# Kernel optimization log

Measured on AMD Instinct MI355X. Metric: run time of the kernel, lower is better.

## Reference

```python
import jax, jax.numpy as jnp
import numpy as np

TAU = 2.0        # LIF membrane time constant
ALPHA = 4.0      # spikingjelly default Sigmoid surrogate alpha
NUM_HEADS = 8

@jax.custom_vjp
def spike(x):
    return (x >= 0.0).astype(x.dtype)

def _spike_fwd(x):
    return spike(x), x

def _spike_bwd(x, g):
    s = jax.nn.sigmoid(ALPHA * x)
    return (g * ALPHA * s * (1.0 - s),)

spike.defvjp(_spike_fwd, _spike_bwd)

def lif(x_seq, v_th):
    """Multi-step LIF over leading time dim. Hard reset to 0, detach_reset."""
    def step(v, xt):
        h = v + (xt - v) / TAU
        s = spike(h - v_th)
        v_new = h * (1.0 - jax.lax.stop_gradient(s))
        return v_new, s
    _, s_seq = jax.lax.scan(step, jnp.zeros_like(x_seq[0]), x_seq)
    return s_seq

def bn_eval(x, w, b, m, v, eps=1e-5):
    # BatchNorm1d in eval mode over channel dim C (last axis here, since the
    # torch code transposes to (TB,C,N) purely to make C the channel axis).
    inv = w / jnp.sqrt(v + eps)
    return x * inv + (b - m * inv)

def setup_inputs() -> dict:
    key = jax.random.key(0)
    T, B, N, C = 4, 8, 512, 512
    ks = jax.random.split(key, 32)
    d = {"x": jax.random.normal(ks[0], (T, B, N, C), dtype=jnp.float32)}
    names = ["q", "k", "v", "p"]
    for i, nm in enumerate(names):
        kk = jax.random.split(ks[i + 1], 6)
        d[nm + "_w"] = jax.random.normal(kk[0], (C, C), dtype=jnp.float32) * (C ** -0.5)
        d[nm + "_b"] = jax.random.normal(kk[1], (C,), dtype=jnp.float32) * 0.01
        d[nm + "_bn_w"] = jax.random.uniform(kk[2], (C,), minval=0.5, maxval=1.5, dtype=jnp.float32)
        d[nm + "_bn_b"] = jax.random.normal(kk[3], (C,), dtype=jnp.float32) * 0.1
        d[nm + "_bn_m"] = jax.random.normal(kk[4], (C,), dtype=jnp.float32) * 0.1
        d[nm + "_bn_v"] = jax.random.uniform(kk[5], (C,), minval=0.5, maxval=1.5, dtype=jnp.float32)
    return d

def _forward(x, q_w, q_b, q_bn_w, q_bn_b, q_bn_m, q_bn_v,
             k_w, k_b, k_bn_w, k_bn_b, k_bn_m, k_bn_v,
             v_w, v_b, v_bn_w, v_bn_b, v_bn_m, v_bn_v,
             p_w, p_b, p_bn_w, p_bn_b, p_bn_m, p_bn_v):
    T, B, N, C = x.shape
    H = NUM_HEADS
    hd = C // H
    scale = hd ** -0.5

    def branch(w, b, bw, bb, bm, bv):
        y = jnp.einsum("tbnc,dc->tbnd", x, w) + b            # Linear
        y = bn_eval(y, bw, bb, bm, bv)                        # BN1d (eval)
        y = lif(y, 1.0)                                       # (T,B,N,C) spikes
        return y.reshape(T, B, N, H, hd).transpose(0, 1, 3, 2, 4)  # (T,B,H,N,hd)

    q = branch(q_w, q_b, q_bn_w, q_bn_b, q_bn_m, q_bn_v)
    k = branch(k_w, k_b, k_bn_w, k_bn_b, k_bn_m, k_bn_v)
    v = branch(v_w, v_b, v_bn_w, v_bn_b, v_bn_m, v_bn_v)

    gamma = 1.0 - 2.0 ** (-5.0 - jnp.arange(H, dtype=jnp.float32))
    idx = jnp.arange(N)
    dist = jnp.abs(idx[:, None] - idx[None, :]).astype(jnp.float32)  # bidirectional
    D = gamma[:, None, None] ** dist                                  # (H,N,N)

    attn = jnp.einsum("tbhnd,tbhmd->tbhnm", q, k) * scale * D
    out = jnp.einsum("tbhnm,tbhmd->tbhnd", attn, v)
    out = out.transpose(0, 1, 3, 2, 4).reshape(T, B, N, C)
    out = lif(out, 0.5)                                      # retention_lif, v_th=0.5

    y = jnp.einsum("tbnc,dc->tbnd", out, p_w) + p_b
    y = bn_eval(y, p_bn_w, p_bn_b, p_bn_m, p_bn_v)
    return lif(y, 1.0)

def reference(x, q_w, q_b, q_bn_w, q_bn_b, q_bn_m, q_bn_v,
              k_w, k_b, k_bn_w, k_bn_b, k_bn_m, k_bn_v,
              v_w, v_b, v_bn_w, v_bn_b, v_bn_m, v_bn_v,
              p_w, p_b, p_bn_w, p_bn_b, p_bn_m, p_bn_v):
    return _forward(x, q_w, q_b, q_bn_w, q_bn_b, q_bn_m, q_bn_v,
                    k_w, k_b, k_bn_w, k_bn_b, k_bn_m, k_bn_v,
                    v_w, v_b, v_bn_w, v_bn_b, v_bn_m, v_bn_v,
                    p_w, p_b, p_bn_w, p_bn_b, p_bn_m, p_bn_v)
```

## Files before the change

kernel.cpp:

```cpp
#include <hip/hip_runtime.h>
#include <cstdint>

typedef unsigned long long u64;

#define TPB 256
#define MARGIN 5e-4
#define FCAP (1 << 20)

typedef __bf16 bf16x8 __attribute__((ext_vector_type(8)));
typedef __bf16 bf16x4 __attribute__((ext_vector_type(4)));
typedef float f32x4 __attribute__((ext_vector_type(4)));

__global__ void init_kernel(double* __restrict__ pw, int* __restrict__ ctr) {
    int h = threadIdx.x;
    if (h < 8) {
        double gamma = 1.0 - ldexp(1.0, -5 - h);
        double p = 1.0;
        for (int i = 0; i < 512; ++i) { pw[h * 512 + i] = p; p *= gamma; }
        ctr[h] = 0;
    }
}

__global__ void split_all(const float* __restrict__ x,
                          const float* __restrict__ w0, const float* __restrict__ w1,
                          const float* __restrict__ w2, const float* __restrict__ w3,
                          __bf16* __restrict__ Xh, __bf16* __restrict__ Xl,
                          __bf16* __restrict__ Wsp) {
    int blk = blockIdx.x;
    if (blk < 8192) {
        size_t i = (size_t)blk * 1024 + threadIdx.x * 4;
        int m = (int)(i >> 9), c = (int)(i & 511);
        int mp = (m & 4095) * 4 + (m >> 12);
        float4 v = *(const float4*)(x + i);
        bf16x4 h4, l4;
        #pragma unroll
        for (int e = 0; e < 4; ++e) {
            float f = (&v.x)[e];
            __bf16 hh = (__bf16)f;
            h4[e] = hh;
            l4[e] = (__bf16)(f - (float)hh);
        }
        size_t dst = (size_t)mp * 512 + c;
        *(bf16x4*)(Xh + dst) = h4;
        *(bf16x4*)(Xl + dst) = l4;
    } else {
        int wb = blk - 8192;
        int br = wb >> 8;
        const float* ws[4] = {w0, w1, w2, w3};
        const float* src = ws[br];
        __bf16* hi = Wsp + (size_t)br * 524288;
        __bf16* lo = hi + 262144;
        size_t i = (size_t)(wb & 255) * 1024 + threadIdx.x * 4;
        float4 v = *(const float4*)(src + i);
        bf16x4 h4, l4;
        #pragma unroll
        for (int e = 0; e < 4; ++e) {
            float f = (&v.x)[e];
            __bf16 hh = (__bf16)f;
            h4[e] = hh;
            l4[e] = (__bf16)(f - (float)hh);
        }
        *(bf16x4*)(hi + i) = h4;
        *(bf16x4*)(lo + i) = l4;
    }
}

__global__ __launch_bounds__(256) void gemm_lif_mask(
    const __bf16* __restrict__ Ahg, const __bf16* __restrict__ Alg,
    const __bf16* __restrict__ Whg, const __bf16* __restrict__ Wlg,
    const float* __restrict__ bias,
    const float* __restrict__ bnw, const float* __restrict__ bnb,
    const float* __restrict__ bnm, const float* __restrict__ bnv,
    u64* __restrict__ msk, int* __restrict__ ctr, int* __restrict__ list, int slot)
{
    __shared__ __bf16 AhS[128][40];
    __shared__ __bf16 AlS[128][40];
    __shared__ __bf16 WhS[128][40];
    __shared__ __bf16 WlS[128][40];

    const int tid = threadIdx.x;
    const int m0 = blockIdx.x * 128;
    const int d0 = blockIdx.y * 128;
    const int wv = tid >> 6;
    const int wm = wv >> 1;
    const int wd = wv & 1;
    const int lane = tid & 63;
    const int fr = lane & 15;
    const int fg = lane >> 4;
    const int srow = tid >> 1;
    const int sseg = (tid & 1) * 16;

    f32x4 acc[4][4];
    #pragma unroll
    for (int i = 0; i < 4; ++i)
        #pragma unroll
        for (int j = 0; j < 4; ++j)
            acc[i][j] = (f32x4){0.f, 0.f, 0.f, 0.f};

    for (int k0 = 0; k0 < 512; k0 += 32) {
        __syncthreads();
        {
            const __bf16* pa = Ahg + (size_t)(m0 + srow) * 512 + k0 + sseg;
            *(bf16x8*)&AhS[srow][sseg]     = *(const bf16x8*)pa;
            *(bf16x8*)&AhS[srow][sseg + 8] = *(const bf16x8*)(pa + 8);
            const __bf16* pl = Alg + (size_t)(m0 + srow) * 512 + k0 + sseg;
            *(bf16x8*)&AlS[srow][sseg]     = *(const bf16x8*)pl;
            *(bf16x8*)&AlS[srow][sseg + 8] = *(const bf16x8*)(pl + 8);
            const __bf16* pwh = Whg + (size_t)(d0 + srow) * 512 + k0 + sseg;
            const __bf16* pwl = Wlg + (size_t)(d0 + srow) * 512 + k0 + sseg;
            *(bf16x8*)&WhS[srow][sseg]     = *(const bf16x8*)pwh;
            *(bf16x8*)&WhS[srow][sseg + 8] = *(const bf16x8*)(pwh + 8);
            *(bf16x8*)&WlS[srow][sseg]     = *(const bf16x8*)pwl;
            *(bf16x8*)&WlS[srow][sseg + 8] = *(const bf16x8*)(pwl + 8);
        }
        __syncthreads();

        bf16x8 ah[4], bh[4], bl[4];
        #pragma unroll
        for (int i = 0; i < 4; ++i)
            ah[i] = *(const bf16x8*)&AhS[wm * 64 + i * 16 + fr][fg * 8];
        #pragma unroll
        for (int j = 0; j < 4; ++j) {
            bh[j] = *(const bf16x8*)&WhS[wd * 64 + j * 16 + fr][fg * 8];
            bl[j] = *(const bf16x8*)&WlS[wd * 64 + j * 16 + fr][fg * 8];
        }
        #pragma unroll
        for (int i = 0; i < 4; ++i)
            #pragma unroll
            for (int j = 0; j < 4; ++j) {
                acc[i][j] = __builtin_amdgcn_mfma_f32_16x16x32_bf16(ah[i], bh[j], acc[i][j], 0, 0, 0);
                acc[i][j] = __builtin_amdgcn_mfma_f32_16x16x32_bf16(ah[i], bl[j], acc[i][j], 0, 0, 0);
            }
        bf16x8 al[4];
        #pragma unroll
        for (int i = 0; i < 4; ++i)
            al[i] = *(const bf16x8*)&AlS[wm * 64 + i * 16 + fr][fg * 8];
        #pragma unroll
        for (int i = 0; i < 4; ++i)
            #pragma unroll
            for (int j = 0; j < 4; ++j)
                acc[i][j] = __builtin_amdgcn_mfma_f32_16x16x32_bf16(al[i], bh[j], acc[i][j], 0, 0, 0);
    }

    double invj[4], shj[4], bsj[4];
    #pragma unroll
    for (int j = 0; j < 4; ++j) {
        int d = d0 + wd * 64 + j * 16 + fr;
        invj[j] = (double)bnw[d] / sqrt((double)bnv[d] + 1e-5);
        shj[j]  = (double)bnb[d] - (double)bnm[d] * invj[j];
        bsj[j]  = (double)bias[d];
    }
    int hword = (d0 >> 6) + wd;
    int bn0 = blockIdx.x * 32 + wm * 16;

    #pragma unroll
    for (int i = 0; i < 4; ++i) {
        int bn = bn0 + i * 4 + fg;
        int b = bn >> 9, n = bn & 511;
        u64 w[4] = {0ull, 0ull, 0ull, 0ull};
        #pragma unroll
        for (int j = 0; j < 4; ++j) {
            double v = 0.0;
            bool fl = false;
            #pragma unroll
            for (int t = 0; t < 4; ++t) {
                double y = ((double)acc[i][j][t] + bsj[j]) * invj[j] + shj[j];
                double hh = v + (y - v) * 0.5;
                fl |= fabs(hh - 1.0) < MARGIN;
                bool s = hh >= 1.0;
                u64 blt = __ballot(s);
                w[t] |= ((blt >> (fg * 16)) & 0xFFFFull) << (j * 16);
                v = s ? 0.0 : hh;
            }
            if (fl) {
                int d = d0 + wd * 64 + j * 16 + fr;
                int idx = atomicAdd(ctr + slot, 1);
                if (idx < FCAP) list[idx] = (b << 18) | (n << 9) | d;
            }
        }
        if (fr == 0) {
            #pragma unroll
            for (int t = 0; t < 4; ++t)
                msk[((t * 8 + b) * 8 + hword) * 512 + n] = w[t];
        }
    }
}

__global__ __launch_bounds__(256) void gemm_final_lif(
    const __bf16* __restrict__ Ahg,
    const __bf16* __restrict__ Whg, const __bf16* __restrict__ Wlg,
    const float* __restrict__ bias,
    const float* __restrict__ bnw, const float* __restrict__ bnb,
    const float* __restrict__ bnm, const float* __restrict__ bnv,
    float* __restrict__ out, int* __restrict__ ctr, int* __restrict__ list)
{
    __shared__ __bf16 AhS[128][40];
    __shared__ __bf16 WhS[128][40];
    __shared__ __bf16 WlS[128][40];

    const int tid = threadIdx.x;
    const int m0 = blockIdx.x * 128;
    const int d0 = blockIdx.y * 128;
    const int wv = tid >> 6;
    const int wm = wv >> 1;
    const int wd = wv & 1;
    const int lane = tid & 63;
    const int fr = lane & 15;
    const int fg = lane >> 4;
    const int srow = tid >> 1;
    const int sseg = (tid & 1) * 16;

    f32x4 acc[4][4];
    #pragma unroll
    for (int i = 0; i < 4; ++i)
        #pragma unroll
        for (int j = 0; j < 4; ++j)
            acc[i][j] = (f32x4){0.f, 0.f, 0.f, 0.f};

    for (int k0 = 0; k0 < 512; k0 += 32) {
        __syncthreads();
        {
            const __bf16* pa = Ahg + (size_t)(m0 + srow) * 512 + k0 + sseg;
            *(bf16x8*)&AhS[srow][sseg]     = *(const bf16x8*)pa;
            *(bf16x8*)&AhS[srow][sseg + 8] = *(const bf16x8*)(pa + 8);
            const __bf16* pwh = Whg + (size_t)(d0 + srow) * 512 + k0 + sseg;
            const __bf16* pwl = Wlg + (size_t)(d0 + srow) * 512 + k0 + sseg;
            *(bf16x8*)&WhS[srow][sseg]     = *(const bf16x8*)pwh;
            *(bf16x8*)&WhS[srow][sseg + 8] = *(const bf16x8*)(pwh + 8);
            *(bf16x8*)&WlS[srow][sseg]     = *(const bf16x8*)pwl;
            *(bf16x8*)&WlS[srow][sseg + 8] = *(const bf16x8*)(pwl + 8);
        }
        __syncthreads();

        bf16x8 ah[4], bh[4], bl[4];
        #pragma unroll
        for (int i = 0; i < 4; ++i)
            ah[i] = *(const bf16x8*)&AhS[wm * 64 + i * 16 + fr][fg * 8];
        #pragma unroll
        for (int j = 0; j < 4; ++j) {
            bh[j] = *(const bf16x8*)&WhS[wd * 64 + j * 16 + fr][fg * 8];
            bl[j] = *(const bf16x8*)&WlS[wd * 64 + j * 16 + fr][fg * 8];
        }
        #pragma unroll
        for (int i = 0; i < 4; ++i)
            #pragma unroll
            for (int j = 0; j < 4; ++j) {
                acc[i][j] = __builtin_amdgcn_mfma_f32_16x16x32_bf16(ah[i], bh[j], acc[i][j], 0, 0, 0);
                acc[i][j] = __builtin_amdgcn_mfma_f32_16x16x32_bf16(ah[i], bl[j], acc[i][j], 0, 0, 0);
            }
    }

    double invj[4], shj[4], bsj[4];
    #pragma unroll
    for (int j = 0; j < 4; ++j) {
        int d = d0 + wd * 64 + j * 16 + fr;
        invj[j] = (double)bnw[d] / sqrt((double)bnv[d] + 1e-5);
        shj[j]  = (double)bnb[d] - (double)bnm[d] * invj[j];
        bsj[j]  = (double)bias[d];
    }
    int bn0 = blockIdx.x * 32 + wm * 16;

    #pragma unroll
    for (int i = 0; i < 4; ++i) {
        int bn = bn0 + i * 4 + fg;
        int b = bn >> 9, n = bn & 511;
        #pragma unroll
        for (int j = 0; j < 4; ++j) {
            int d = d0 + wd * 64 + j * 16 + fr;
            double v = 0.0;
            bool fl = false;
            #pragma unroll
            for (int t = 0; t < 4; ++t) {
                double y = ((double)acc[i][j][t] + bsj[j]) * invj[j] + shj[j];
                double hh = v + (y - v) * 0.5;
                fl |= fabs(hh - 1.0) < MARGIN;
                bool s = hh >= 1.0;
                out[((size_t)((t * 8 + b) * 512 + n) << 9) + d] = s ? 1.0f : 0.0f;
                v = s ? 0.0 : hh;
            }
            if (fl) {
                int idx = atomicAdd(ctr + 3, 1);
                if (idx < FCAP) list[idx] = (b << 18) | (n << 9) | d;
            }
        }
    }
}

__global__ void fix_mask(const float* __restrict__ x, const float* __restrict__ w,
                         const float* __restrict__ bias,
                         const float* __restrict__ bnw, const float* __restrict__ bnb,
                         const float* __restrict__ bnm, const float* __restrict__ bnv,
                         u64* __restrict__ msk, const int* __restrict__ ctr,
                         const int* __restrict__ list, int slot) {
    int cnt = ctr[slot]; if (cnt > FCAP) cnt = FCAP;
    int wv = (blockIdx.x * blockDim.x + threadIdx.x) >> 6;
    int nw = (gridDim.x * blockDim.x) >> 6;
    int lane = threadIdx.x & 63;
    for (int i = wv; i < cnt; i += nw) {
        int g = list[i];
        int c = g & 511, n = (g >> 9) & 511, b = g >> 18;
        int h = c >> 6;
        const float* wr = w + (size_t)c * 512;
        double dot[4];
        #pragma unroll
        for (int t = 0; t < 4; ++t) {
            const float* xr = x + ((size_t)((t * 8 + b) * 512 + n) << 9);
            double p = 0.0;
            #pragma unroll
            for (int j = 0; j < 8; ++j)
                p += (double)xr[lane + 64 * j] * (double)wr[lane + 64 * j];
            dot[t] = p;
        }
        #pragma unroll
        for (int off = 32; off; off >>= 1) {
            #pragma unroll
            for (int t = 0; t < 4; ++t)
                dot[t] += __shfl_xor(dot[t], off, 64);
        }
        if (lane == 0) {
            double inv = (double)bnw[c] / sqrt((double)bnv[c] + 1e-5);
            double sh  = (double)bnb[c] - (double)bnm[c] * inv;
            double bs  = (double)bias[c];
            double v = 0.0;
            u64 bit = 1ull << (c & 63);
            for (int t = 0; t < 4; ++t) {
                double y = (dot[t] + bs) * inv + sh;
                double hh = v + (y - v) * 0.5;
                bool s = hh >= 1.0;
                u64* wp_ = &msk[((t * 8 + b) * 8 + h) * 512 + n];
                if (s) atomicOr(wp_, bit); else atomicAnd(wp_, ~bit);
                v = s ? 0.0 : hh;
            }
        }
    }
}

__global__ __launch_bounds__(256) void ret_fused2(
    const u64* __restrict__ qm, const u64* __restrict__ km,
    const u64* __restrict__ vm, const double* __restrict__ pw,
    float* __restrict__ O)
{
    int bid = blockIdx.x;
    int tbh = bid >> 3;
    int n0 = (bid & 7) * 64;
    int h = tbh & 7;
    int tb = tbh >> 3;
    int tid = threadIdx.x;
    int wv = tid >> 6, lane = tid & 63, fr = lane & 15, fg = lane >> 4;
    int wn = wv * 16;

    __shared__ __bf16 Ks[64][72];
    __shared__ u64 VsTg[16][66];
    __shared__ u64 ShTg[4][16][17];
    __shared__ u64 SlTg[4][16][17];
    __shared__ u64 vmc[64];
    __shared__ float pwf[512];

    int base = tbh * 512;
    for (int i = tid; i < 512; i += 256) pwf[i] = (float)pw[h * 512 + i] * 0.125f;

    union U8 { u64 q[2]; bf16x8 v; };

    u64 qw = qm[base + n0 + wn + fr];
    bf16x8 qf[2];
    #pragma unroll
    for (int ks = 0; ks < 2; ++ks) {
        int e0 = ks * 32 + fg * 8;
        u64 plo = 0, phi = 0;
        #pragma unroll
        for (int e = 0; e < 4; ++e) {
            if ((qw >> (e0 + e)) & 1ull)     plo |= 0x3F80ull << (16 * e);
            if ((qw >> (e0 + 4 + e)) & 1ull) phi |= 0x3F80ull << (16 * e);
        }
        U8 u; u.q[0] = plo; u.q[1] = phi; qf[ks] = u.v;
    }

    f32x4 acc_o[4];
    #pragma unroll
    for (int j = 0; j < 4; ++j) acc_o[j] = (f32x4){0.f, 0.f, 0.f, 0.f};

    int nglob = n0 + wn + fr;

    for (int mc = 0; mc < 8; ++mc) {
        __syncthreads();
        {
            int row = tid >> 2, q4 = (tid & 3) * 16;
            u64 kw = km[base + mc * 64 + row];
            #pragma unroll
            for (int s = 0; s < 4; ++s) {
                int e0 = q4 + s * 4;
                u64 pk = 0;
                #pragma unroll
                for (int e = 0; e < 4; ++e)
                    if ((kw >> (e0 + e)) & 1ull) pk |= 0x3F80ull << (16 * e);
                *(u64*)&Ks[row][e0] = pk;
            }
        }
        if (tid < 64) vmc[tid] = vm[base + mc * 64 + tid];
        __syncthreads();
        {
            #pragma unroll
            for (int c = 0; c < 4; ++c) {
                int mg = wv * 4 + c;
                u64 pk = 0;
                #pragma unroll
                for (int e = 0; e < 4; ++e)
                    if ((vmc[mg * 4 + e] >> lane) & 1ull) pk |= 0x3F80ull << (16 * e);
                VsTg[mg][lane] = pk;
            }
        }
        f32x4 accs[4];
        #pragma unroll
        for (int j = 0; j < 4; ++j) accs[j] = (f32x4){0.f, 0.f, 0.f, 0.f};
        #pragma unroll
        for (int ks = 0; ks < 2; ++ks) {
            #pragma unroll
            for (int j = 0; j < 4; ++j) {
                bf16x8 ka = *(const bf16x8*)&Ks[j * 16 + fr][ks * 32 + fg * 8];
                accs[j] = __builtin_amdgcn_mfma_f32_16x16x32_bf16(ka, qf[ks], accs[j], 0, 0, 0);
            }
        }
        #pragma unroll
        for (int j = 0; j < 4; ++j) {
            u64 ph = 0, pl = 0;
            #pragma unroll
            for (int reg = 0; reg < 4; ++reg) {
                int m = mc * 64 + j * 16 + fg * 4 + reg;
                int dist = nglob - m; if (dist < 0) dist = -dist;
                float a = accs[j][reg] * pwf[dist];
                __bf16 hp = (__bf16)a;
                __bf16 lp = (__bf16)(a - (float)hp);
                ph |= (u64)__builtin_bit_cast(unsigned short, hp) << (16 * reg);
                pl |= (u64)__builtin_bit_cast(unsigned short, lp) << (16 * reg);
            }
            ShTg[wv][j * 4 + fg][fr] = ph;
            SlTg[wv][j * 4 + fg][fr] = pl;
        }
        __syncthreads();
        #pragma unroll
        for (int ks2 = 0; ks2 < 2; ++ks2) {
            int mga = ks2 * 8 + fg * 2;
            U8 ua, ul;
            ua.q[0] = ShTg[wv][mga][fr];  ua.q[1] = ShTg[wv][mga + 1][fr];
            ul.q[0] = SlTg[wv][mga][fr];  ul.q[1] = SlTg[wv][mga + 1][fr];
            #pragma unroll
            for (int j2 = 0; j2 < 4; ++j2) {
                U8 uv;
                uv.q[0] = VsTg[mga][j2 * 16 + fr];
                uv.q[1] = VsTg[mga + 1][j2 * 16 + fr];
                acc_o[j2] = __builtin_amdgcn_mfma_f32_16x16x32_bf16(ua.v, uv.v, acc_o[j2], 0, 0, 0);
                acc_o[j2] = __builtin_amdgcn_mfma_f32_16x16x32_bf16(ul.v, uv.v, acc_o[j2], 0, 0, 0);
            }
        }
    }

    #pragma unroll
    for (int j2 = 0; j2 < 4; ++j2) {
        int c = h * 64 + j2 * 16 + fr;
        #pragma unroll
        for (int reg = 0; reg < 4; ++reg) {
            int n = n0 + wn + fg * 4 + reg;
            O[((size_t)(tb * 512 + n) << 9) + c] = acc_o[j2][reg];
        }
    }
}

__global__ void lif_ret_bf2(const float* __restrict__ Y, __bf16* __restrict__ Rb,
                            int* __restrict__ ctr, int* __restrict__ list) {
    int g = blockIdx.x * TPB + threadIdx.x;
    int c = g & 511, n = (g >> 9) & 511, b = g >> 18;
    size_t pbase = ((size_t)(b * 512 + n) * 4) * 512 + c;
    double v = 0.0, eb = 0.0;
    bool flag = false;
    for (int t = 0; t < 4; ++t) {
        size_t idx = ((size_t)((t * 8 + b) * 512 + n) << 9) + c;
        double x = (double)Y[idx];
        double hh = v + (x - v) * 0.5;
        eb = 0.5 * eb + 0.5 * (fabs(x) * 1e-4);
        flag |= fabs(hh - 0.5) <= eb + 1e-9;
        bool s = hh >= 0.5;
        Rb[pbase + (size_t)t * 512] = s ? (__bf16)1.0f : (__bf16)0.0f;
        v = s ? 0.0 : hh;
        if (s) eb = 0.0;
    }
    if (flag) {
        int i2 = atomicAdd(ctr + 4, 1);
        if (i2 < FCAP) list[i2] = g;
    }
}

__global__ void repair_ret_bf2(const u64* __restrict__ qm, const u64* __restrict__ km,
                               const u64* __restrict__ vm, const double* __restrict__ pw,
                               const int* __restrict__ ctr, const int* __restrict__ list,
                               __bf16* __restrict__ Rb) {
    int cnt = ctr[4]; if (cnt > FCAP) cnt = FCAP;
    int wv = (blockIdx.x * blockDim.x + threadIdx.x) >> 6;
    int nw = (gridDim.x * blockDim.x) >> 6;
    int lane = threadIdx.x & 63;
    for (int i = wv; i < cnt; i += nw) {
        int g = list[i];
        int c = g & 511, n = (g >> 9) & 511, b = g >> 18;
        int h = c >> 6, d = c & 63;
        double acc_t[4];
        for (int t = 0; t < 4; ++t) {
            int base = ((t * 8 + b) * 8 + h) * 512;
            u64 qw = qm[base + n];
            double p = 0.0;
            for (int j = 0; j < 8; ++j) {
                int m = j * 64 + lane;
                u64 kk = km[base + m];
                u64 vvm = vm[base + m];
                if ((vvm >> d) & 1ull) {
                    int dist = n - m; if (dist < 0) dist = -dist;
                    p += (double)__popcll(qw & kk) * pw[h * 512 + dist];
                }
            }
            acc_t[t] = p;
        }
        #pragma unroll
        for (int off = 32; off; off >>= 1) {
            #pragma unroll
            for (int t = 0; t < 4; ++t) acc_t[t] += __shfl_xor(acc_t[t], off, 64);
        }
        if (lane == 0) {
            double v = 0.0;
            size_t pbase = ((size_t)(b * 512 + n) * 4) * 512 + c;
            for (int t = 0; t < 4; ++t) {
                double x = acc_t[t] * 0.125;
                double hh = v + (x - v) * 0.5;
                bool s = hh >= 0.5;
                Rb[pbase + (size_t)t * 512] = s ? (__bf16)1.0f : (__bf16)0.0f;
                v = s ? 0.0 : hh;
            }
        }
    }
}

__global__ void fix_final_direct(const __bf16* __restrict__ rr, const float* __restrict__ w,
                                 const float* __restrict__ bias,
                                 const float* __restrict__ bnw, const float* __restrict__ bnb,
                                 const float* __restrict__ bnm, const float* __restrict__ bnv,
                                 const int* __restrict__ ctr, const int* __restrict__ list,
                                 float* __restrict__ out) {
    int cnt = ctr[3]; if (cnt > FCAP) cnt = FCAP;
    int wv = (blockIdx.x * blockDim.x + threadIdx.x) >> 6;
    int nw = (gridDim.x * blockDim.x) >> 6;
    int lane = threadIdx.x & 63;
    for (int i = wv; i < cnt; i += nw) {
        int g = list[i];
        int c = g & 511, n = (g >> 9) & 511, b = g >> 18;
        const float* wr = w + (size_t)c * 512;
        double dot[4];
        #pragma unroll
        for (int t = 0; t < 4; ++t) {
            const __bf16* xr = rr + ((size_t)(b * 512 + n) * 4 + t) * 512;
            double p = 0.0;
            #pragma unroll
            for (int j = 0; j < 8; ++j)
                p += (double)(float)xr[lane + 64 * j] * (double)wr[lane + 64 * j];
            dot[t] = p;
        }
        #pragma unroll
        for (int off = 32; off; off >>= 1) {
            #pragma unroll
            for (int t = 0; t < 4; ++t)
                dot[t] += __shfl_xor(dot[t], off, 64);
        }
        if (lane == 0) {
            double inv = (double)bnw[c] / sqrt((double)bnv[c] + 1e-5);
            double sh  = (double)bnb[c] - (double)bnm[c] * inv;
            double bs  = (double)bias[c];
            double v = 0.0;
            for (int t = 0; t < 4; ++t) {
                double y = (dot[t] + bs) * inv + sh;
                double hh = v + (y - v) * 0.5;
                bool s = hh >= 1.0;
                out[((size_t)((t * 8 + b) * 512 + n) << 9) + c] = s ? 1.0f : 0.0f;
                v = s ? 0.0 : hh;
            }
        }
    }
}

__global__ __launch_bounds__(256) void gemm_bn_mfma(
    const float* __restrict__ A, const float* __restrict__ W,
    const float* __restrict__ bias,
    const float* __restrict__ bnw, const float* __restrict__ bnb,
    const float* __restrict__ bnm, const float* __restrict__ bnv,
    float* __restrict__ out)
{
    __shared__ __bf16 Ah[128][36];
    __shared__ __bf16 Al[128][36];
    __shared__ __bf16 Wh[64][36];
    __shared__ __bf16 Wl[64][36];

    const int tid = threadIdx.x;
    const int m0 = blockIdx.x * 128;
    const int d0 = blockIdx.y * 64;
    const int wv = tid >> 6;
    const int wm = wv >> 1;
    const int wd = wv & 1;
    const int lane = tid & 63;
    const int fr = lane & 15;
    const int fg = lane >> 4;
    const int srow = tid >> 3;
    const int scol = (tid & 7) * 4;

    f32x4 acc[4][2];
    #pragma unroll
    for (int i = 0; i < 4; ++i)
        #pragma unroll
        for (int j = 0; j < 2; ++j)
            acc[i][j] = (f32x4){0.f, 0.f, 0.f, 0.f};

    for (int k0 = 0; k0 < 512; k0 += 32) {
        __syncthreads();
        #pragma unroll
        for (int rep = 0; rep < 4; ++rep) {
            int row = srow + 32 * rep;
            float4 va = *(const float4*)(A + (size_t)(m0 + row) * 512 + k0 + scol);
            #pragma unroll
            for (int e = 0; e < 4; ++e) {
                float f = (&va.x)[e];
                __bf16 h = (__bf16)f;
                Ah[row][scol + e] = h;
                Al[row][scol + e] = (__bf16)(f - (float)h);
            }
        }
        #pragma unroll
        for (int rep = 0; rep < 2; ++rep) {
            int row = srow + 32 * rep;
            float4 vw = *(const float4*)(W + (size_t)(d0 + row) * 512 + k0 + scol);
            #pragma unroll
            for (int e = 0; e < 4; ++e) {
                float f = (&vw.x)[e];
                __bf16 h = (__bf16)f;
                Wh[row][scol + e] = h;
                Wl[row][scol + e] = (__bf16)(f - (float)h);
            }
        }
        __syncthreads();

        union FU { bf16x8 v8; struct { __bf16 a[4], b[4]; } s; };
        bf16x8 ah[4], al[4], bh[2], bl[2];
        #pragma unroll
        for (int i = 0; i < 4; ++i) {
            int row = wm * 64 + i * 16 + fr;
            FU u1, u2;
            *(double*)&u1.s.a[0] = *(const double*)&Ah[row][fg * 8];
            *(double*)&u1.s.b[0] = *(const double*)&Ah[row][fg * 8 + 4];
            *(double*)&u2.s.a[0] = *(const double*)&Al[row][fg * 8];
            *(double*)&u2.s.b[0] = *(const double*)&Al[row][fg * 8 + 4];
            ah[i] = u1.v8; al[i] = u2.v8;
        }
        #pragma unroll
        for (int j = 0; j < 2; ++j) {
            int row = wd * 32 + j * 16 + fr;
            FU u1, u2;
            *(double*)&u1.s.a[0] = *(const double*)&Wh[row][fg * 8];
            *(double*)&u1.s.b[0] = *(const double*)&Wh[row][fg * 8 + 4];
            *(double*)&u2.s.a[0] = *(const double*)&Wl[row][fg * 8];
            *(double*)&u2.s.b[0] = *(const double*)&Wl[row][fg * 8 + 4];
            bh[j] = u1.v8; bl[j] = u2.v8;
        }
        #pragma unroll
        for (int i = 0; i < 4; ++i)
            #pragma unroll
            for (int j = 0; j < 2; ++j) {
                acc[i][j] = __builtin_amdgcn_mfma_f32_16x16x32_bf16(ah[i], bh[j], acc[i][j], 0, 0, 0);
                acc[i][j] = __builtin_amdgcn_mfma_f32_16x16x32_bf16(ah[i], bl[j], acc[i][j], 0, 0, 0);
                acc[i][j] = __builtin_amdgcn_mfma_f32_16x16x32_bf16(al[i], bh[j], acc[i][j], 0, 0, 0);
            }
    }

    #pragma unroll
    for (int j = 0; j < 2; ++j) {
        int d = d0 + wd * 32 + j * 16 + fr;
        double inv = (double)bnw[d] / sqrt((double)bnv[d] + 1e-5);
        double sh  = (double)bnb[d] - (double)bnm[d] * inv;
        double bs  = (double)bias[d];
        #pragma unroll
        for (int i = 0; i < 4; ++i) {
            #pragma unroll
            for (int reg = 0; reg < 4; ++reg) {
                int m = m0 + wm * 64 + i * 16 + fg * 4 + reg;
                out[(size_t)m * 512 + d] = (float)(((double)acc[i][j][reg] + bs) * inv + sh);
            }
        }
    }
}

__global__ void lif_mask_flag(const float* __restrict__ Y, u64* __restrict__ msk,
                              int* __restrict__ ctr, int* __restrict__ list, int slot) {
    int g = blockIdx.x * TPB + threadIdx.x;
    int c = g & 511, n = (g >> 9) & 511, b = g >> 18;
    int h = c >> 6;
    int lane = threadIdx.x & 63;
    double v = 0.0;
    bool flag = false;
    for (int t = 0; t < 4; ++t) {
        float y = Y[((size_t)((t * 8 + b) * 512 + n) << 9) + c];
        double hh = v + ((double)y - v) * 0.5;
        flag |= fabs(hh - 1.0) < MARGIN;
        bool s = hh >= 1.0;
        u64 mk = __ballot(s);
        if (lane == 0) msk[((t * 8 + b) * 8 + h) * 512 + n] = mk;
        v = s ? 0.0 : hh;
    }
    if (flag) {
        int idx = atomicAdd(ctr + slot, 1);
        if (idx < FCAP) list[idx] = g;
    }
}

__global__ void lif_ret_f(const float* __restrict__ Y, float* __restrict__ R,
                          int* __restrict__ ctr, int* __restrict__ list) {
    int g = blockIdx.x * TPB + threadIdx.x;
    int c = g & 511, n = (g >> 9) & 511, b = g >> 18;
    double v = 0.0, eb = 0.0;
    bool flag = false;
    for (int t = 0; t < 4; ++t) {
        size_t idx = ((size_t)((t * 8 + b) * 512 + n) << 9) + c;
        double x = (double)Y[idx];
        double hh = v + (x - v) * 0.5;
        eb = 0.5 * eb + 0.5 * (fabs(x) * 1e-4);
        flag |= fabs(hh - 0.5) <= eb + 1e-9;
        bool s = hh >= 0.5;
        R[idx] = s ? 1.0f : 0.0f;
        v = s ? 0.0 : hh;
        if (s) eb = 0.0;
    }
    if (flag) {
        int i2 = atomicAdd(ctr + 4, 1);
        if (i2 < FCAP) list[i2] = g;
    }
}

__global__ void repair_ret_f(const u64* __restrict__ qm, const u64* __restrict__ km,
                             const u64* __restrict__ vm, const double* __restrict__ pw,
                             const int* __restrict__ ctr, const int* __restrict__ list,
                             float* __restrict__ r) {
    int cnt = ctr[4]; if (cnt > FCAP) cnt = FCAP;
    int wv = (blockIdx.x * blockDim.x + threadIdx.x) >> 6;
    int nw = (gridDim.x * blockDim.x) >> 6;
    int lane = threadIdx.x & 63;
    for (int i = wv; i < cnt; i += nw) {
        int g = list[i];
        int c = g & 511, n = (g >> 9) & 511, b = g >> 18;
        int h = c >> 6, d = c & 63;
        double acc_t[4];
        for (int t = 0; t < 4; ++t) {
            int base = ((t * 8 + b) * 8 + h) * 512;
            u64 qw = qm[base + n];
            double p = 0.0;
            for (int j = 0; j < 8; ++j) {
                int m = j * 64 + lane;
                u64 kk = km[base + m];
                u64 vvm = vm[base + m];
                if ((vvm >> d) & 1ull) {
                    int dist = n - m; if (dist < 0) dist = -dist;
                    p += (double)__popcll(qw & kk) * pw[h * 512 + dist];
                }
            }
            acc_t[t] = p;
        }
        #pragma unroll
        for (int off = 32; off; off >>= 1) {
            #pragma unroll
            for (int t = 0; t < 4; ++t) acc_t[t] += __shfl_xor(acc_t[t], off, 64);
        }
        if (lane == 0) {
            double v = 0.0;
            for (int t = 0; t < 4; ++t) {
                double x = acc_t[t] * 0.125;
                double hh = v + (x - v) * 0.5;
                bool s = hh >= 0.5;
                r[((size_t)((t * 8 + b) * 512 + n) << 9) + c] = s ? 1.0f : 0.0f;
                v = s ? 0.0 : hh;
            }
        }
    }
}

__global__ void final_flag(const float* __restrict__ Y, int* __restrict__ ctr,
                           int* __restrict__ list) {
    int g = blockIdx.x * TPB + threadIdx.x;
    int c = g & 511, n = (g >> 9) & 511, b = g >> 18;
    double v = 0.0;
    bool flag = false;
    for (int t = 0; t < 4; ++t) {
        float y = Y[((size_t)((t * 8 + b) * 512 + n) << 9) + c];
        double hh = v + ((double)y - v) * 0.5;
        flag |= fabs(hh - 1.0) < MARGIN;
        bool s = hh >= 1.0;
        v = s ? 0.0 : hh;
    }
    if (flag) {
        int idx = atomicAdd(ctr + 3, 1);
        if (idx < FCAP) list[idx] = g;
    }
}

__global__ void fix_final_f(const float* __restrict__ rr, const float* __restrict__ w,
                            const float* __restrict__ bias,
                            const float* __restrict__ bnw, const float* __restrict__ bnb,
                            const float* __restrict__ bnm, const float* __restrict__ bnv,
                            const int* __restrict__ ctr, int* __restrict__ list) {
    int cnt = ctr[3]; if (cnt > FCAP) cnt = FCAP;
    int wv = (blockIdx.x * blockDim.x + threadIdx.x) >> 6;
    int nw = (gridDim.x * blockDim.x) >> 6;
    int lane = threadIdx.x & 63;
    for (int i = wv; i < cnt; i += nw) {
        int g = list[i] & 0x00FFFFFF;
        int c = g & 511, n = (g >> 9) & 511, b = g >> 18;
        const float* wr = w + (size_t)c * 512;
        double dot[4];
        #pragma unroll
        for (int t = 0; t < 4; ++t) {
            const float* xr = rr + ((size_t)((t * 8 + b) * 512 + n) << 9);
            double p = 0.0;
            #pragma unroll
            for (int j = 0; j < 8; ++j)
                p += (double)xr[lane + 64 * j] * (double)wr[lane + 64 * j];
            dot[t] = p;
        }
        #pragma unroll
        for (int off = 32; off; off >>= 1) {
            #pragma unroll
            for (int t = 0; t < 4; ++t)
                dot[t] += __shfl_xor(dot[t], off, 64);
        }
        if (lane == 0) {
            double inv = (double)bnw[c] / sqrt((double)bnv[c] + 1e-5);
            double sh  = (double)bnb[c] - (double)bnm[c] * inv;
            double bs  = (double)bias[c];
            double v = 0.0;
            int sp = 0;
            for (int t = 0; t < 4; ++t) {
                double y = (dot[t] + bs) * inv + sh;
                double hh = v + (y - v) * 0.5;
                bool s = hh >= 1.0;
                sp |= (s ? 1 : 0) << t;
                v = s ? 0.0 : hh;
            }
            list[i] = g | (sp << 24);
        }
    }
}

__global__ void final_write(const float* __restrict__ Y, float* __restrict__ out) {
    int g = blockIdx.x * TPB + threadIdx.x;
    int c = g & 511, n = (g >> 9) & 511, b = g >> 18;
    double v = 0.0;
    for (int t = 0; t < 4; ++t) {
        size_t idx = ((size_t)((t * 8 + b) * 512 + n) << 9) + c;
        float y = Y[idx];
        double hh = v + ((double)y - v) * 0.5;
        bool s = hh >= 1.0;
        out[idx] = s ? 1.0f : 0.0f;
        v = s ? 0.0 : hh;
    }
}

__global__ void fix_scatter(const int* __restrict__ ctr, const int* __restrict__ list,
                            float* __restrict__ out) {
    int cnt = ctr[3]; if (cnt > FCAP) cnt = FCAP;
    int i = blockIdx.x * blockDim.x + threadIdx.x;
    if (i >= cnt) return;
    int e = list[i];
    int g = e & 0x00FFFFFF, sp = (e >> 24) & 0xF;
    int c = g & 511, n = (g >> 9) & 511, b = g >> 18;
    for (int t = 0; t < 4; ++t)
        out[((size_t)((t * 8 + b) * 512 + n) << 9) + c] = ((sp >> t) & 1) ? 1.0f : 0.0f;
}

extern "C" void kernel_launch(void* const* d_in, const int* in_sizes, int n_in,
                              void* d_out, int out_size, void* d_ws, size_t ws_size,
                              hipStream_t stream) {
    const float* x = (const float*)d_in[0];
    const float *w[4], *bi[4], *bnw[4], *bnb[4], *bnm[4], *bnv[4];
    for (int br = 0; br < 4; ++br) {
        int base = 1 + br * 6;
        w[br]   = (const float*)d_in[base + 0];
        bi[br]  = (const float*)d_in[base + 1];
        bnw[br] = (const float*)d_in[base + 2];
        bnb[br] = (const float*)d_in[base + 3];
        bnm[br] = (const float*)d_in[base + 4];
        bnv[br] = (const float*)d_in[base + 5];
    }

    const size_t NX = (size_t)16384 * 512;
    char* p = (char*)d_ws;
    double* pw = (double*)p;  p += 8 * 512 * sizeof(double);
    u64* qm = (u64*)p;        p += 131072 * sizeof(u64);
    u64* km = (u64*)p;        p += 131072 * sizeof(u64);
    u64* vm = (u64*)p;        p += 131072 * sizeof(u64);
    int* ctr = (int*)p;       p += 1024;
    int* list = (int*)p;      p += (size_t)FCAP * sizeof(int);
    float* Y = (float*)p;     p += NX * 4;
    __bf16* Xh = (__bf16*)p;  p += NX * 2;
    __bf16* Xl = (__bf16*)p;  p += NX * 2;
    __bf16* Wsp = (__bf16*)p; p += (size_t)4 * 2 * 262144 * 2;
    size_t need_fast = (size_t)(p - (char*)d_ws);
    int fast = ws_size >= need_fast;

    init_kernel<<<1, 64, 0, stream>>>(pw, ctr);

    dim3 g2(128, 4);
    dim3 gg(128, 8);

    if (fast) {
        split_all<<<8192 + 1024, 256, 0, stream>>>(x, w[0], w[1], w[2], w[3], Xh, Xl, Wsp);
        for (int br = 0; br < 3; ++br) {
            u64* msk = br == 0 ? qm : (br == 1 ? km : vm);
            gemm_lif_mask<<<g2, 256, 0, stream>>>(Xh, Xl,
                Wsp + (size_t)br * 524288, Wsp + (size_t)br * 524288 + 262144,
                bi[br], bnw[br], bnb[br], bnm[br], bnv[br], msk, ctr, list, br);
            fix_mask<<<128, 256, 0, stream>>>(x, w[br], bi[br], bnw[br], bnb[br],
                                              bnm[br], bnv[br], msk, ctr, list, br);
        }
        ret_fused2<<<2048, 256, 0, stream>>>(qm, km, vm, pw, Y);
        lif_ret_bf2<<<8192, TPB, 0, stream>>>(Y, Xh, ctr, list);
        repair_ret_bf2<<<256, 256, 0, stream>>>(qm, km, vm, pw, ctr, list, Xh);
        gemm_final_lif<<<g2, 256, 0, stream>>>(Xh,
            Wsp + (size_t)3 * 524288, Wsp + (size_t)3 * 524288 + 262144,
            bi[3], bnw[3], bnb[3], bnm[3], bnv[3], (float*)d_out, ctr, list);
        fix_final_direct<<<128, 256, 0, stream>>>(Xh, w[3], bi[3], bnw[3], bnb[3],
                                                  bnm[3], bnv[3], ctr, list, (float*)d_out);
    } else {
        for (int br = 0; br < 3; ++br) {
            u64* msk = br == 0 ? qm : (br == 1 ? km : vm);
            gemm_bn_mfma<<<gg, 256, 0, stream>>>(x, w[br], bi[br], bnw[br], bnb[br],
                                                 bnm[br], bnv[br], Y);
            lif_mask_flag<<<8192, TPB, 0, stream>>>(Y, msk, ctr, list, br);
            fix_mask<<<128, 256, 0, stream>>>(x, w[br], bi[br], bnw[br], bnb[br],
                                              bnm[br], bnv[br], msk, ctr, list, br);
        }
        float* r = (float*)d_out;
        ret_fused2<<<2048, 256, 0, stream>>>(qm, km, vm, pw, Y);
        lif_ret_f<<<8192, TPB, 0, stream>>>(Y, r, ctr, list);
        repair_ret_f<<<256, 256, 0, stream>>>(qm, km, vm, pw, ctr, list, r);
        gemm_bn_mfma<<<gg, 256, 0, stream>>>(r, w[3], bi[3], bnw[3], bnb[3],
                                             bnm[3], bnv[3], Y);
        final_flag<<<8192, TPB, 0, stream>>>(Y, ctr, list);
        fix_final_f<<<128, 256, 0, stream>>>(r, w[3], bi[3], bnw[3], bnb[3],
                                             bnm[3], bnv[3], ctr, list);
        final_write<<<8192, TPB, 0, stream>>>(Y, (float*)d_out);
        fix_scatter<<<4096, 256, 0, stream>>>(ctr, list, (float*)d_out);
    }
}
```

Baseline: 282.5 us.

## Use direct global-to-LDS loads with XOR-swizzled shared tiles in GEMMs

The two projection GEMM kernels now stage tiles with global_load_lds, which writes global data straight into shared memory without going through registers. The padded 40-wide shared arrays become unpadded 32-wide arrays with an XOR swizzle on the column index to avoid bank conflicts, and the fragment reads apply the same swizzle. The attention kernel's hi/lo bf16 split now truncates the high half by masking bits instead of rounding, which changes the split but keeps hi+lo close to the value. The aim is fewer staging instructions and lower register pressure, at the risk of getting the swizzle mapping wrong.

```diff
diff --git a/kernel.cpp b/kernel.cpp
--- a/kernel.cpp
+++ b/kernel.cpp
@@ -10,6 +10,13 @@
 typedef __bf16 bf16x8 __attribute__((ext_vector_type(8)));
 typedef __bf16 bf16x4 __attribute__((ext_vector_type(4)));
 typedef float f32x4 __attribute__((ext_vector_type(4)));
+
+typedef __attribute__((address_space(1))) void GV;
+typedef __attribute__((address_space(3))) void LV;
+typedef __attribute__((address_space(3))) char LC;
+
+#define GLD(gsrc, ldst) __builtin_amdgcn_global_load_lds( \
+    (GV*)(void*)(gsrc), (LV*)(ldst), 16, 0, 0)
 
 __global__ void init_kernel(double* __restrict__ pw, int* __restrict__ ctr) {
     int h = threadIdx.x;
@@ -73,10 +80,10 @@
     const float* __restrict__ bnm, const float* __restrict__ bnv,
     u64* __restrict__ msk, int* __restrict__ ctr, int* __restrict__ list, int slot)
 {
-    __shared__ __bf16 AhS[128][40];
-    __shared__ __bf16 AlS[128][40];
-    __shared__ __bf16 WhS[128][40];
-    __shared__ __bf16 WlS[128][40];
+    __shared__ __bf16 AhS[128][32];
+    __shared__ __bf16 AlS[128][32];
+    __shared__ __bf16 WhS[128][32];
+    __shared__ __bf16 WlS[128][32];
 
     const int tid = threadIdx.x;
     const int m0 = blockIdx.x * 128;
@@ -87,8 +94,26 @@
     const int lane = tid & 63;
     const int fr = lane & 15;
     const int fg = lane >> 4;
-    const int srow = tid >> 1;
-    const int sseg = (tid & 1) * 16;
+
+    const int lr   = lane >> 2;
+    const int csrc = (lane & 3) ^ ((lane >> 3) & 3);
+    const int rA0  = wv * 32 + lr;
+    const __bf16* gAh0 = Ahg + (size_t)(m0 + rA0) * 512 + csrc * 8;
+    const __bf16* gAh1 = gAh0 + (size_t)16 * 512;
+    const __bf16* gAl0 = Alg + (size_t)(m0 + rA0) * 512 + csrc * 8;
+    const __bf16* gAl1 = gAl0 + (size_t)16 * 512;
+    const __bf16* gWh0 = Whg + (size_t)(d0 + rA0) * 512 + csrc * 8;
+    const __bf16* gWh1 = gWh0 + (size_t)16 * 512;
+    const __bf16* gWl0 = Wlg + (size_t)(d0 + rA0) * 512 + csrc * 8;
+    const __bf16* gWl1 = gWl0 + (size_t)16 * 512;
+
+    unsigned ldsOff = __builtin_amdgcn_readfirstlane((unsigned)(wv * 2048));
+    LC* lAh = (LC*)(LV*)&AhS[0][0] + ldsOff;
+    LC* lAl = (LC*)(LV*)&AlS[0][0] + ldsOff;
+    LC* lWh = (LC*)(LV*)&WhS[0][0] + ldsOff;
+    LC* lWl = (LC*)(LV*)&WlS[0][0] + ldsOff;
+
+    const int fcol = (fg ^ ((fr >> 1) & 3)) * 16;
 
     f32x4 acc[4][4];
     #pragma unroll
@@ -99,30 +124,23 @@
 
     for (int k0 = 0; k0 < 512; k0 += 32) {
         __syncthreads();
-        {
-            const __bf16* pa = Ahg + (size_t)(m0 + srow) * 512 + k0 + sseg;
-            *(bf16x8*)&AhS[srow][sseg]     = *(const bf16x8*)pa;
-            *(bf16x8*)&AhS[srow][sseg + 8] = *(const bf16x8*)(pa + 8);
-            const __bf16* pl = Alg + (size_t)(m0 + srow) * 512 + k0 + sseg;
-            *(bf16x8*)&AlS[srow][sseg]     = *(const bf16x8*)pl;
-            *(bf16x8*)&AlS[srow][sseg + 8] = *(const bf16x8*)(pl + 8);
-            const __bf16* pwh = Whg + (size_t)(d0 + srow) * 512 + k0 + sseg;
-            const __bf16* pwl = Wlg + (size_t)(d0 + srow) * 512 + k0 + sseg;
-            *(bf16x8*)&WhS[srow][sseg]     = *(const bf16x8*)pwh;
-            *(bf16x8*)&WhS[srow][sseg + 8] = *(const bf16x8*)(pwh + 8);
-            *(bf16x8*)&WlS[srow][sseg]     = *(const bf16x8*)pwl;
-            *(bf16x8*)&WlS[srow][sseg + 8] = *(const bf16x8*)(pwl + 8);
-        }
+        GLD(gAh0 + k0, lAh); GLD(gAh1 + k0, lAh + 1024);
+        GLD(gAl0 + k0, lAl); GLD(gAl1 + k0, lAl + 1024);
+        GLD(gWh0 + k0, lWh); GLD(gWh1 + k0, lWh + 1024);
+        GLD(gWl0 + k0, lWl); GLD(gWl1 + k0, lWl + 1024);
         __syncthreads();
 
         bf16x8 ah[4], bh[4], bl[4];
         #pragma unroll
-        for (int i = 0; i < 4; ++i)
-            ah[i] = *(const bf16x8*)&AhS[wm * 64 + i * 16 + fr][fg * 8];
+        for (int i = 0; i < 4; ++i) {
+            int row = wm * 64 + i * 16 + fr;
+            ah[i] = *(const bf16x8*)((const char*)&AhS[0][0] + row * 64 + fcol);
+        }
         #pragma unroll
         for (int j = 0; j < 4; ++j) {
-            bh[j] = *(const bf16x8*)&WhS[wd * 64 + j * 16 + fr][fg * 8];
-            bl[j] = *(const bf16x8*)&WlS[wd * 64 + j * 16 + fr][fg * 8];
+            int row = wd * 64 + j * 16 + fr;
+            bh[j] = *(const bf16x8*)((const char*)&WhS[0][0] + row * 64 + fcol);
+            bl[j] = *(const bf16x8*)((const char*)&WlS[0][0] + row * 64 + fcol);
         }
         #pragma unroll
         for (int i = 0; i < 4; ++i)
@@ -133,8 +151,10 @@
             }
         bf16x8 al[4];
         #pragma unroll
-        for (int i = 0; i < 4; ++i)
-            al[i] = *(const bf16x8*)&AlS[wm * 64 + i * 16 + fr][fg * 8];
+        for (int i = 0; i < 4; ++i) {
+            int row = wm * 64 + i * 16 + fr;
+            al[i] = *(const bf16x8*)((const char*)&AlS[0][0] + row * 64 + fcol);
+        }
         #pragma unroll
         for (int i = 0; i < 4; ++i)
             #pragma unroll
@@ -194,9 +214,9 @@
     const float* __restrict__ bnm, const float* __restrict__ bnv,
     float* __restrict__ out, int* __restrict__ ctr, int* __restrict__ list)
 {
-    __shared__ __bf16 AhS[128][40];
-    __shared__ __bf16 WhS[128][40];
-    __shared__ __bf16 WlS[128][40];
+    __shared__ __bf16 AhS[128][32];
+    __shared__ __bf16 WhS[128][32];
+    __shared__ __bf16 WlS[128][32];
 
     const int tid = threadIdx.x;
     const int m0 = blockIdx.x * 128;
@@ -207,8 +227,23 @@
     const int lane = tid & 63;
     const int fr = lane & 15;
     const int fg = lane >> 4;
-    const int srow = tid >> 1;
-    const int sseg = (tid & 1) * 16;
+
+    const int lr   = lane >> 2;
+    const int csrc = (lane & 3) ^ ((lane >> 3) & 3);
+    const int rA0  = wv * 32 + lr;
+    const __bf16* gAh0 = Ahg + (size_t)(m0 + rA0) * 512 + csrc * 8;
+    const __bf16* gAh1 = gAh0 + (size_t)16 * 512;
+    const __bf16* gWh0 = Whg + (size_t)(d0 + rA0) * 512 + csrc * 8;
+    const __bf16* gWh1 = gWh0 + (size_t)16 * 512;
+    const __bf16* gWl0 = Wlg + (size_t)(d0 + rA0) * 512 + csrc * 8;
+    const __bf16* gWl1 = gWl0 + (size_t)16 * 512;
+
+    unsigned ldsOff = __builtin_amdgcn_readfirstlane((unsigned)(wv * 2048));
+    LC* lAh = (LC*)(LV*)&AhS[0][0] + ldsOff;
+    LC* lWh = (LC*)(LV*)&WhS[0][0] + ldsOff;
+    LC* lWl = (LC*)(LV*)&WlS[0][0] + ldsOff;
+
+    const int fcol = (fg ^ ((fr >> 1) & 3)) * 16;
 
     f32x4 acc[4][4];
     #pragma unroll
@@ -219,27 +254,22 @@
 
     for (int k0 = 0; k0 < 512; k0 += 32) {
         __syncthreads();
-        {
-            const __bf16* pa = Ahg + (size_t)(m0 + srow) * 512 + k0 + sseg;
-            *(bf16x8*)&AhS[srow][sseg]     = *(const bf16x8*)pa;
-            *(bf16x8*)&AhS[srow][sseg + 8] = *(const bf16x8*)(pa + 8);
-            const __bf16* pwh = Whg + (size_t)(d0 + srow) * 512 + k0 + sseg;
-            const __bf16* pwl = Wlg + (size_t)(d0 + srow) * 512 + k0 + sseg;
-            *(bf16x8*)&WhS[srow][sseg]     = *(const bf16x8*)pwh;
-            *(bf16x8*)&WhS[srow][sseg + 8] = *(const bf16x8*)(pwh + 8);
-            *(bf16x8*)&WlS[srow][sseg]     = *(const bf16x8*)pwl;
-            *(bf16x8*)&WlS[srow][sseg + 8] = *(const bf16x8*)(pwl + 8);
-        }
+        GLD(gAh0 + k0, lAh); GLD(gAh1 + k0, lAh + 1024);
+        GLD(gWh0 + k0, lWh); GLD(gWh1 + k0, lWh + 1024);
+        GLD(gWl0 + k0, lWl); GLD(gWl1 + k0, lWl + 1024);
         __syncthreads();
 
         bf16x8 ah[4], bh[4], bl[4];
         #pragma unroll
-        for (int i = 0; i < 4; ++i)
-            ah[i] = *(const bf16x8*)&AhS[wm * 64 + i * 16 + fr][fg * 8];
+        for (int i = 0; i < 4; ++i) {
+            int row = wm * 64 + i * 16 + fr;
+            ah[i] = *(const bf16x8*)((const char*)&AhS[0][0] + row * 64 + fcol);
+        }
         #pragma unroll
         for (int j = 0; j < 4; ++j) {
-            bh[j] = *(const bf16x8*)&WhS[wd * 64 + j * 16 + fr][fg * 8];
-            bl[j] = *(const bf16x8*)&WlS[wd * 64 + j * 16 + fr][fg * 8];
+            int row = wd * 64 + j * 16 + fr;
+            bh[j] = *(const bf16x8*)((const char*)&WhS[0][0] + row * 64 + fcol);
+            bl[j] = *(const bf16x8*)((const char*)&WlS[0][0] + row * 64 + fcol);
         }
         #pragma unroll
         for (int i = 0; i < 4; ++i)
@@ -428,10 +458,12 @@
                 int m = mc * 64 + j * 16 + fg * 4 + reg;
                 int dist = nglob - m; if (dist < 0) dist = -dist;
                 float a = accs[j][reg] * pwf[dist];
-                __bf16 hp = (__bf16)a;
-                __bf16 lp = (__bf16)(a - (float)hp);
-                ph |= (u64)__builtin_bit_cast(unsigned short, hp) << (16 * reg);
-                pl |= (u64)__builtin_bit_cast(unsigned short, lp) << (16 * reg);
+                unsigned ab = __builtin_bit_cast(unsigned, a);
+                unsigned hb = ab & 0xFFFF0000u;
+                float lp = a - __builtin_bit_cast(float, hb);
+                __bf16 lpb = (__bf16)lp;
+                ph |= (u64)(ab >> 16) << (16 * reg);
+                pl |= (u64)__builtin_bit_cast(unsigned short, lpb) << (16 * reg);
             }
             ShTg[wv][j * 4 + fg][fr] = ph;
             SlTg[wv][j * 4 + fg][fr] = pl;
```

Measured after the change: 277.3 us (median of 2 runs). No clear change (-1.9%).
